# Optimization experiments

Measured on AMD Instinct MI355X. Metric: run time of the kernel, lower is better.

## Reference

```python
import jax, jax.numpy as jnp
import numpy as np

B, T, C = 4, 1024, 1024
H, G = 16, 1            # n_head, n_query_groups
D = C // H              # head_dim = 64
E, K = 4, 1             # moe_num_experts, moe_k
FF = 4 * C              # ffn/expert hidden = 4096
EPS = 1e-5


def setup_inputs() -> dict:
    key = jax.random.key(0)
    ks = jax.random.split(key, 24)
    w = lambda k, shape: (jax.random.normal(k, shape, jnp.float32) * 0.02)
    return {
        "x": jax.random.normal(ks[0], (B, T, C), jnp.float32),
        # attention (torch Linear weights stored as [in, out])
        "wq": w(ks[1], (C, C)), "wk": w(ks[2], (C, C)), "wv": w(ks[3], (C, C)),
        "wo": w(ks[4], (C, C)), "bo": jnp.zeros((C,), jnp.float32),
        # feedforward
        "ff_w1": w(ks[5], (C, FF)), "ff_b1": jnp.zeros((FF,), jnp.float32),
        "ff_w2": w(ks[6], (FF, C)), "ff_b2": jnp.zeros((C,), jnp.float32),
        # MoE experts (stacked) + gate
        "exp_w1": w(ks[7], (E, C, FF)), "exp_b1": jnp.zeros((E, FF), jnp.float32),
        "exp_w2": w(ks[8], (E, FF, C)), "exp_b2": jnp.zeros((E, C), jnp.float32),
        "gate_w": w(ks[9], (C, E)), "gate_b": jnp.zeros((E,), jnp.float32),
        # layernorms
        "ln1_g": jnp.ones((C,), jnp.float32), "ln1_b": jnp.zeros((C,), jnp.float32),
        "ln2_g": jnp.ones((C,), jnp.float32), "ln2_b": jnp.zeros((C,), jnp.float32),
        "ln3_g": jnp.ones((C,), jnp.float32), "ln3_b": jnp.zeros((C,), jnp.float32),
    }


def _ln(x, g, b):
    m = x.mean(-1, keepdims=True)
    v = x.var(-1, keepdims=True)
    return (x - m) / jnp.sqrt(v + EPS) * g + b


def reference(x, wq, wk, wv, wo, bo, ff_w1, ff_b1, ff_w2, ff_b2,
              exp_w1, exp_b1, exp_w2, exp_b2, gate_w, gate_b,
              ln1_g, ln1_b, ln2_g, ln2_b, ln3_g, ln3_b):
    Hg = H // G
    # ---- grouped-query causal self-attention ----
    h = _ln(x, ln1_g, ln1_b)
    # [B,T,C] -> [B,G,Hg,T,D]
    q = (h @ wq).reshape(B, T, G, Hg, D).transpose(0, 2, 3, 1, 4)
    k = (h @ wk).reshape(B, T, G, Hg, D).transpose(0, 2, 3, 1, 4)
    v = (h @ wv).reshape(B, T, G, Hg, D).transpose(0, 2, 3, 1, 4)
    scores = jnp.einsum('bghtd,bghsd->bghts', q, k) / np.float32(np.sqrt(D))
    causal = jnp.tril(jnp.ones((T, T), bool))
    scores = jnp.where(causal, scores, -jnp.inf)
    probs = jax.nn.softmax(scores, axis=-1)
    o = jnp.einsum('bghts,bghsd->bghtd', probs, v)          # [B,G,Hg,T,D]
    o = o.reshape(B, H, T, D).transpose(0, 2, 1, 3).reshape(B, T, C)
    x = x + o @ wo + bo
    # ---- dense feedforward ----
    h = _ln(x, ln2_g, ln2_b)
    x = x + jax.nn.relu(h @ ff_w1 + ff_b1) @ ff_w2 + ff_b2
    # ---- MoE: compute ALL experts densely, gather top-k (faithful to source) ----
    h = _ln(x, ln3_g, ln3_b)
    gate = h @ gate_w + gate_b                               # [B,T,E]
    topk_s, topk_i = jax.lax.top_k(gate, K)                  # [B,T,K]
    topk_w = jax.nn.softmax(topk_s, axis=-1)
    hidden = jax.nn.relu(jnp.einsum('btc,ech->bteh', h, exp_w1) + exp_b1)
    expert_out = jnp.einsum('bteh,ehc->btec', hidden, exp_w2) + exp_b2  # [B,T,E,C]
    sel = jnp.take_along_axis(expert_out, topk_i[..., None], axis=2)    # [B,T,K,C]
    moe = (sel * topk_w[..., None]).sum(axis=2)
    return x + moe
```

## Files before the change

### kernel.cpp

```cpp
#include <hip/hip_runtime.h>


using f16   = _Float16;
using f16x4 = __attribute__((ext_vector_type(4))) _Float16;
using f16x8 = __attribute__((ext_vector_type(8))) _Float16;
using f32x4 = __attribute__((ext_vector_type(4))) float;

__device__ __forceinline__ void async16(void* l, const void* g) {
  __builtin_amdgcn_global_load_lds(
      (const __attribute__((address_space(1))) unsigned*)g,
      (__attribute__((address_space(3))) unsigned*)l, 16, 0, 0);
}

template <bool SPLITW>
__global__ __launch_bounds__(256) void transpose_k(
    const float* __restrict__ in, f16* __restrict__ oh, f16* __restrict__ ol,
    int R, int Cc) {
  const size_t bofs = (size_t)blockIdx.y * R * Cc;
  in += bofs; oh += bofs;
  if constexpr (SPLITW) ol += bofs;
  __shared__ float tile[32][33];
  const int nbx = Cc >> 5;
  const int bx = blockIdx.x % nbx, by = blockIdx.x / nbx;
  const int tx = threadIdx.x & 31, ty = threadIdx.x >> 5;
#pragma unroll
  for (int i = 0; i < 4; ++i) {
    int r = ty + i * 8;
    tile[r][tx] = in[(size_t)(by * 32 + r) * Cc + bx * 32 + tx];
  }
  __syncthreads();
#pragma unroll
  for (int i = 0; i < 4; ++i) {
    int oc = ty + i * 8;
    float v = tile[tx][oc];
    size_t o = (size_t)(bx * 32 + oc) * R + by * 32 + tx;
    f16 hi = (f16)v;
    oh[o] = hi;
    if constexpr (SPLITW) ol[o] = (f16)(v - (float)hi);
  }
}

__global__ __launch_bounds__(256) void ln_k(
    const float* __restrict__ x, const float* __restrict__ g,
    const float* __restrict__ b, f16* __restrict__ outh, f16* __restrict__ outl) {
  const int row = blockIdx.x;
  const float4 vv = ((const float4*)(x + (size_t)row * 1024))[threadIdx.x];
  float s = vv.x + vv.y + vv.z + vv.w;
  float sq = vv.x * vv.x + vv.y * vv.y + vv.z * vv.z + vv.w * vv.w;
#pragma unroll
  for (int mm = 32; mm; mm >>= 1) { s += __shfl_xor(s, mm); sq += __shfl_xor(sq, mm); }
  __shared__ float red[8];
  const int wv = threadIdx.x >> 6;
  if ((threadIdx.x & 63) == 0) { red[wv] = s; red[4 + wv] = sq; }
  __syncthreads();
  s = red[0] + red[1] + red[2] + red[3];
  sq = red[4] + red[5] + red[6] + red[7];
  const float mean = s * 0.0009765625f;
  const float rstd = rsqrtf(sq * 0.0009765625f - mean * mean + 1e-5f);
  const int c = threadIdx.x * 4;
  const float xs[4] = {vv.x, vv.y, vv.z, vv.w};
  f16x4 ovh, ovl;
#pragma unroll
  for (int i = 0; i < 4; ++i) {
    float val = (xs[i] - mean) * rstd * g[c + i] + b[c + i];
    f16 hi = (f16)val;
    ovh[i] = hi;
    ovl[i] = (f16)(val - (float)hi);
  }
  *(f16x4*)(outh + (size_t)row * 1024 + c) = ovh;
  *(f16x4*)(outl + (size_t)row * 1024 + c) = ovl;
}

__global__ __launch_bounds__(256) void gate_k(
    const float* __restrict__ x, const float* __restrict__ g, const float* __restrict__ b,
    const float* __restrict__ gw, const float* __restrict__ gb,
    int* __restrict__ cnt, int* __restrict__ idxAll, int* __restrict__ eid) {
  const int t = blockIdx.x;
  const float4 vv = ((const float4*)(x + (size_t)t * 1024))[threadIdx.x];
  float s = vv.x + vv.y + vv.z + vv.w;
  float sq = vv.x * vv.x + vv.y * vv.y + vv.z * vv.z + vv.w * vv.w;
#pragma unroll
  for (int mm = 32; mm; mm >>= 1) { s += __shfl_xor(s, mm); sq += __shfl_xor(sq, mm); }
  __shared__ float red[8];
  __shared__ float redv[4][4];
  const int wv = threadIdx.x >> 6;
  if ((threadIdx.x & 63) == 0) { red[wv] = s; red[4 + wv] = sq; }
  __syncthreads();
  s = red[0] + red[1] + red[2] + red[3];
  sq = red[4] + red[5] + red[6] + red[7];
  const float mean = s * 0.0009765625f;
  const float rstd = rsqrtf(sq * 0.0009765625f - mean * mean + 1e-5f);
  const int c = threadIdx.x * 4;
  const float xs[4] = {vv.x, vv.y, vv.z, vv.w};
  float a0 = 0.f, a1 = 0.f, a2 = 0.f, a3 = 0.f;
#pragma unroll
  for (int i = 0; i < 4; ++i) {
    float ln = (xs[i] - mean) * rstd * g[c + i] + b[c + i];
    const float4 w4 = ((const float4*)gw)[c + i];
    a0 += ln * w4.x; a1 += ln * w4.y; a2 += ln * w4.z; a3 += ln * w4.w;
  }
#pragma unroll
  for (int mm = 32; mm; mm >>= 1) {
    a0 += __shfl_xor(a0, mm); a1 += __shfl_xor(a1, mm);
    a2 += __shfl_xor(a2, mm); a3 += __shfl_xor(a3, mm);
  }
  if ((threadIdx.x & 63) == 0) {
    redv[wv][0] = a0; redv[wv][1] = a1; redv[wv][2] = a2; redv[wv][3] = a3;
  }
  __syncthreads();
  if (threadIdx.x == 0) {
    float ge[4];
#pragma unroll
    for (int e = 0; e < 4; ++e)
      ge[e] = redv[0][e] + redv[1][e] + redv[2][e] + redv[3][e] + gb[e];
    int be = 0; float bvv = ge[0];
#pragma unroll
    for (int e = 1; e < 4; ++e) if (ge[e] > bvv) { bvv = ge[e]; be = e; }
    int pos = atomicAdd(&cnt[be], 1);
    idxAll[(be << 12) + pos] = t;
    eid[t] = be;
  }
}

__global__ void init_moe(int* cnt) { if (threadIdx.x < 4) cnt[threadIdx.x] = 0; }

#define MAXMT 36
__global__ void plan_k(const int* __restrict__ cnt, int* __restrict__ desc) {
  if (threadIdx.x == 0) {
    int t = 0;
    for (int e = 0; e < 4; ++e) {
      const int c = cnt[e];
      for (int m = 0; m < c; m += 128) desc[t++] = (e << 16) | (m >> 7);
    }
    for (; t < MAXMT; ++t) desc[t] = -1;
  }
}

template <bool MOE>
__global__ __launch_bounds__(256) void reduce_k(
    const float* __restrict__ p0, const float* __restrict__ p1,
    const float* __restrict__ res, const float* __restrict__ bias,
    const int* __restrict__ eid, float* __restrict__ o) {
  const int row = blockIdx.x, t = threadIdx.x;
  const float* bp = MOE ? bias + (size_t)eid[row] * 1024 : bias;
  const float4 a = ((const float4*)(p0 + (size_t)row * 1024))[t];
  const float4 b = ((const float4*)(p1 + (size_t)row * 1024))[t];
  const float4 r = ((const float4*)(res + (size_t)row * 1024))[t];
  const float4 bb = ((const float4*)bp)[t];
  float4 o4;
  o4.x = r.x + a.x + b.x + bb.x;
  o4.y = r.y + a.y + b.y + bb.y;
  o4.z = r.z + a.z + b.z + bb.z;
  o4.w = r.w + a.w + b.w + bb.w;
  ((float4*)(o + (size_t)row * 1024))[t] = o4;
}

template <bool SPLIT, bool RELU, bool BIAS, bool RES, bool GATHER, int OUT,
          bool QKV3, bool KSPLIT>
__global__ __launch_bounds__(256, 2) void gemm_k(
    const f16* __restrict__ Ah, const f16* __restrict__ Al,
    const f16* __restrict__ Bh, const f16* __restrict__ Bl,
    float* __restrict__ outf, float* __restrict__ outf2,
    f16* __restrict__ outh, f16* __restrict__ outl,
    const float* __restrict__ bias, const float* __restrict__ res,
    const int* __restrict__ idxAll, const int* __restrict__ cntAll,
    const int* __restrict__ desc,
    int M, int N, int K) {
  const int NB = N >> 7;
  int m0, n0, ks = 0;
  int cnt = M;
  const int* idx = nullptr;
  if constexpr (GATHER) {
    int rem = blockIdx.x;
    if constexpr (KSPLIT) {
      const int half = (int)gridDim.x >> 1;
      ks = rem >= half; rem -= ks * half;
    }
    const int mt = rem / NB, nt = rem - mt * NB;
    const int d = desc[mt];
    if (d < 0) return;
    const int e = d >> 16;
    m0 = (d & 0xffff) << 7;
    n0 = nt << 7;
    cnt = cntAll[e];
    idx = idxAll + (e << 12);
    Bh += (size_t)e * N * K;
    if (BIAS) bias += (size_t)e * N;
  } else {
    int rem = blockIdx.x;
    const int ntile = (int)gridDim.x >> (KSPLIT ? 1 : 0);
    if constexpr (KSPLIT) { ks = rem >= ntile; rem -= ks * ntile; }
    const int q2 = ntile >> 3;
    const int bid = (rem & 7) * q2 + (rem >> 3);
    m0 = (bid / NB) << 7; n0 = (bid % NB) << 7;
  }

  __shared__ __align__(16) char lds[65536];

  const int tid = threadIdx.x;
  const int wave = tid >> 6, lane = tid & 63;
  const int wr = (wave >> 1) << 6, wc = (wave & 1) << 6;
  const int srow = lane >> 3;
  const int lc = (lane & 7) ^ srow;
  const int kofs = (SPLIT ? (lc >> 1) : lc) << 4;

  const int kshift = (KSPLIT && ks) ? (K >> 1) : 0;

  const char* srcA[4];
  const char* srcB[4];
#pragma unroll
  for (int s = 0; s < 4; ++s) {
    const int tr = (wave * 4 + s) * 8 + srow;
    int gm = m0 + tr;
    if constexpr (GATHER) gm = idx[gm < cnt ? gm : cnt - 1];
    const f16* baseA = (SPLIT && (lc & 1)) ? Al : Ah;
    srcA[s] = (const char*)baseA + ((size_t)gm * K + kshift) * 2 + kofs;
    const f16* baseB = (SPLIT && (lc & 1)) ? Bl : Bh;
    srcB[s] = (const char*)baseB + ((size_t)(n0 + tr) * K + kshift) * 2 + kofs;
  }
  char* const ldsw = lds + wave * 4096;

  const int s4 = lane >> 4, l7 = lane & 7, fr = lane & 15;
  int offAh[4], offAl[4], offBh[4], offBl[4];
#pragma unroll
  for (int i = 0; i < 4; ++i) {
    const int row = wr + i * 16 + fr;
    const int col = wc + i * 16 + fr;
    if constexpr (SPLIT) {
      offAh[i] = row * 128 + (((2 * s4) ^ l7) << 4);
      offAl[i] = row * 128 + (((2 * s4 + 1) ^ l7) << 4);
      offBh[i] = 16384 + col * 128 + (((2 * s4) ^ l7) << 4);
      offBl[i] = 16384 + col * 128 + (((2 * s4 + 1) ^ l7) << 4);
    } else {
      offAh[i] = row * 128 + ((s4 ^ l7) << 4);
      offAl[i] = row * 128 + (((4 + s4) ^ l7) << 4);
      offBh[i] = 16384 + col * 128 + ((s4 ^ l7) << 4);
      offBl[i] = 16384 + col * 128 + (((4 + s4) ^ l7) << 4);
    }
  }

  f32x4 acc[4][4] = {};

  constexpr int KSTEP = SPLIT ? 32 : 64;
  const int nt_ = (KSPLIT ? (K >> 1) : K) / KSTEP;

#pragma unroll
  for (int s = 0; s < 4; ++s) {
    async16(ldsw + s * 1024, srcA[s]);
    async16(ldsw + 16384 + s * 1024, srcB[s]);
  }

  for (int t = 0; t < nt_; ++t) {
    const int cur = t & 1;
    if (t + 1 < nt_) {
      const size_t kb = (size_t)(t + 1) * (KSTEP * 2);
      char* dst = ldsw + (cur ^ 1) * 32768;
#pragma unroll
      for (int s = 0; s < 4; ++s) {
        async16(dst + s * 1024, srcA[s] + kb);
        async16(dst + 16384 + s * 1024, srcB[s] + kb);
      }
      asm volatile("s_waitcnt vmcnt(8)" ::: "memory");
    } else {
      asm volatile("s_waitcnt vmcnt(0)" ::: "memory");
    }
    __builtin_amdgcn_s_barrier();
    __builtin_amdgcn_sched_barrier(0);

    const char* cab = lds + cur * 32768;
    f16x8 va[4], vb[4], va2[4], vb2[4];
#pragma unroll
    for (int i = 0; i < 4; ++i) {
      va[i]  = *(const f16x8*)(cab + offAh[i]);
      va2[i] = *(const f16x8*)(cab + offAl[i]);
      vb[i]  = *(const f16x8*)(cab + offBh[i]);
      vb2[i] = *(const f16x8*)(cab + offBl[i]);
    }
    __builtin_amdgcn_s_setprio(1);
#pragma unroll
    for (int i = 0; i < 4; ++i)
#pragma unroll
      for (int j = 0; j < 4; ++j) {
        if constexpr (SPLIT) {
          acc[i][j] = __builtin_amdgcn_mfma_f32_16x16x32_f16(va[i],  vb[j],  acc[i][j], 0, 0, 0);
          acc[i][j] = __builtin_amdgcn_mfma_f32_16x16x32_f16(va2[i], vb[j],  acc[i][j], 0, 0, 0);
          acc[i][j] = __builtin_amdgcn_mfma_f32_16x16x32_f16(va[i],  vb2[j], acc[i][j], 0, 0, 0);
        } else {
          acc[i][j] = __builtin_amdgcn_mfma_f32_16x16x32_f16(va[i],  vb[j],  acc[i][j], 0, 0, 0);
          acc[i][j] = __builtin_amdgcn_mfma_f32_16x16x32_f16(va2[i], vb2[j], acc[i][j], 0, 0, 0);
        }
      }
    __builtin_amdgcn_s_setprio(0);
    __builtin_amdgcn_sched_barrier(0);
    __builtin_amdgcn_s_barrier();
  }

  const int cl = lane & 15, rg = lane >> 4;
  float* const po = (OUT == 3) ? (ks ? outf2 : outf) : outf;
#pragma unroll
  for (int i = 0; i < 4; ++i) {
#pragma unroll
    for (int r = 0; r < 4; ++r) {
      const int mloc = m0 + wr + i * 16 + rg * 4 + r;
      if (GATHER && mloc >= cnt) continue;
      const int orow = GATHER ? idx[mloc] : mloc;
#pragma unroll
      for (int j = 0; j < 4; ++j) {
        const int col = n0 + wc + j * 16 + cl;
        float v2 = acc[i][j][r];
        if (BIAS) v2 += bias[col];
        if (RELU) v2 = v2 > 0.f ? v2 : 0.f;
        if (RES) v2 += res[(size_t)orow * N + col];
        size_t oidx;
        if constexpr (QKV3) oidx = ((size_t)(col >> 10) * M + orow) * 1024 + (col & 1023);
        else oidx = (size_t)orow * N + col;
        if constexpr (OUT == 0 || OUT == 3) {
          po[oidx] = v2;
        } else if constexpr (OUT == 1) {
          f16 hi = (f16)v2;
          outh[oidx] = hi;
          outl[oidx] = (f16)(v2 - (float)hi);
        } else {
          outh[oidx] = (f16)v2;
        }
      }
    }
  }
}

__global__ __launch_bounds__(256, 2) void attn_k(
    const f16* __restrict__ qh, const f16* __restrict__ ql,
    const f16* __restrict__ kh, const f16* __restrict__ kl,
    const f16* __restrict__ vh, const f16* __restrict__ vl,
    f16* __restrict__ oh, f16* __restrict__ ol) {
  const int qt = blockIdx.x & 15, hd = (blockIdx.x >> 4) & 15, bb = blockIdx.x >> 8;
  const int tid = threadIdx.x, wave = tid >> 6, lane = tid & 63;
  __shared__ __align__(16) char Qs[16384], Ks[16384], Vs[16384], Ps[16384];
  const int swz = (((lane & 7) ^ ((lane >> 3) & 7)) << 4);
  const size_t tok0 = (size_t)bb * 1024;
  const int hoff = hd * 64;
  const float L2E = 1.44269504089f;

#pragma unroll
  for (int r = 0; r < 2; ++r) {
    const int chunk = wave * 2 + r;
    const int row = chunk * 8 + (lane >> 3);
    const size_t byte = (((tok0 + qt * 64 + row) * 1024 + hoff) << 1) + swz;
    async16(Qs + chunk * 1024, (const char*)qh + byte);
    async16(Qs + 8192 + chunk * 1024, (const char*)ql + byte);
  }

  f32x4 oacc[4] = {};
  float mrun[4] = {-1e30f, -1e30f, -1e30f, -1e30f};
  float lrun[4] = {};

  for (int kt = 0; kt <= qt; ++kt) {
    __syncthreads();
#pragma unroll
    for (int r = 0; r < 2; ++r) {
      const int chunk = wave * 2 + r;
      const int row = chunk * 8 + (lane >> 3);
      const size_t byte = (((tok0 + kt * 64 + row) * 1024 + hoff) << 1) + swz;
      async16(Ks + chunk * 1024, (const char*)kh + byte);
      async16(Ks + 8192 + chunk * 1024, (const char*)kl + byte);
    }
    {
      const int kv = tid >> 2, d0 = (tid & 3) << 4;
      const size_t vbase = (tok0 + kt * 64 + kv) * 1024 + hoff + d0;
      f16x8 a0 = *(const f16x8*)(vh + vbase);
      f16x8 a1 = *(const f16x8*)(vh + vbase + 8);
      f16x8 c0 = *(const f16x8*)(vl + vbase);
      f16x8 c1 = *(const f16x8*)(vl + vbase + 8);
#pragma unroll
      for (int jj = 0; jj < 8; ++jj) {
        const int d = d0 + jj, d2 = d0 + 8 + jj;
        const int o1 = d * 128 + ((kv * 2) ^ ((d & 7) << 4));
        const int o2 = d2 * 128 + ((kv * 2) ^ ((d2 & 7) << 4));
        *(f16*)(Vs + o1) = a0[jj]; *(f16*)(Vs + 8192 + o1) = c0[jj];
        *(f16*)(Vs + o2) = a1[jj]; *(f16*)(Vs + 8192 + o2) = c1[jj];
      }
    }
    __syncthreads();

    f32x4 s[4] = {};
#pragma unroll
    for (int ks = 0; ks < 2; ++ks) {
      const int qrow = wave * 16 + (lane & 15);
      const int qoff = qrow * 128 + ((((ks << 2) + (lane >> 4)) ^ (qrow & 7)) << 4);
      f16x8 a_h = *(const f16x8*)(Qs + qoff);
      f16x8 a_l = *(const f16x8*)(Qs + 8192 + qoff);
#pragma unroll
      for (int j = 0; j < 4; ++j) {
        const int col = j * 16 + (lane & 15);
        const int koff = col * 128 + ((((ks << 2) + (lane >> 4)) ^ (col & 7)) << 4);
        f16x8 b_h = *(const f16x8*)(Ks + koff);
        f16x8 b_l = *(const f16x8*)(Ks + 8192 + koff);
        s[j] = __builtin_amdgcn_mfma_f32_16x16x32_f16(a_h, b_h, s[j], 0, 0, 0);
        s[j] = __builtin_amdgcn_mfma_f32_16x16x32_f16(a_l, b_h, s[j], 0, 0, 0);
        s[j] = __builtin_amdgcn_mfma_f32_16x16x32_f16(a_h, b_l, s[j], 0, 0, 0);
      }
    }

    const bool diag = (kt == qt);
    float pmax[4] = {-1e30f, -1e30f, -1e30f, -1e30f};
#pragma unroll
    for (int j = 0; j < 4; ++j)
#pragma unroll
      for (int r = 0; r < 4; ++r) {
        float sv = s[j][r] * 0.125f;
        if (diag) {
          const int qloc = wave * 16 + (lane >> 4) * 4 + r;
          const int kvl = j * 16 + (lane & 15);
          if (kvl > qloc) sv = -1e30f;
        }
        s[j][r] = sv;
        pmax[r] = fmaxf(pmax[r], sv);
      }
    char* pbh = Ps + wave * 2048;
    char* pbl = Ps + 8192 + wave * 2048;
#pragma unroll
    for (int r = 0; r < 4; ++r) {
#pragma unroll
      for (int mm = 1; mm < 16; mm <<= 1)
        pmax[r] = fmaxf(pmax[r], __shfl_xor(pmax[r], mm, 16));
      const float mnew = fmaxf(mrun[r], pmax[r]);
      const float al = exp2f((mrun[r] - mnew) * L2E);
      mrun[r] = mnew;
      lrun[r] *= al;
      oacc[0][r] *= al; oacc[1][r] *= al; oacc[2][r] *= al; oacc[3][r] *= al;
    }

    float psum[4] = {};
#pragma unroll
    for (int j = 0; j < 4; ++j)
#pragma unroll
      for (int r = 0; r < 4; ++r) {
        const float p = exp2f((s[j][r] - mrun[r]) * L2E);
        psum[r] += p;
        const int lr = (lane >> 4) * 4 + r;
        const int kvl = j * 16 + (lane & 15);
        const int poff = lr * 128 + ((kvl * 2) ^ ((lr & 7) << 4));
        f16 ph = (f16)p;
        *(f16*)(pbh + poff) = ph;
        *(f16*)(pbl + poff) = (f16)(p - (float)ph);
      }
#pragma unroll
    for (int r = 0; r < 4; ++r) {
#pragma unroll
      for (int mm = 1; mm < 16; mm <<= 1)
        psum[r] += __shfl_xor(psum[r], mm, 16);
      lrun[r] += psum[r];
    }

#pragma unroll
    for (int ks = 0; ks < 2; ++ks) {
      const int prow = lane & 15;
      const int poff = prow * 128 + ((((ks << 2) + (lane >> 4)) ^ (prow & 7)) << 4);
      f16x8 a_h = *(const f16x8*)(pbh + poff);
      f16x8 a_l = *(const f16x8*)(pbl + poff);
#pragma unroll
      for (int jd = 0; jd < 4; ++jd) {
        const int col = jd * 16 + (lane & 15);
        const int voff = col * 128 + ((((ks << 2) + (lane >> 4)) ^ (col & 7)) << 4);
        f16x8 b_h = *(const f16x8*)(Vs + voff);
        f16x8 b_l = *(const f16x8*)(Vs + 8192 + voff);
        oacc[jd] = __builtin_amdgcn_mfma_f32_16x16x32_f16(a_h, b_h, oacc[jd], 0, 0, 0);
        oacc[jd] = __builtin_amdgcn_mfma_f32_16x16x32_f16(a_l, b_h, oacc[jd], 0, 0, 0);
        oacc[jd] = __builtin_amdgcn_mfma_f32_16x16x32_f16(a_h, b_l, oacc[jd], 0, 0, 0);
      }
    }
  }

#pragma unroll
  for (int r = 0; r < 4; ++r) {
    const float inv = 1.0f / lrun[r];
    const size_t trow = tok0 + qt * 64 + wave * 16 + (lane >> 4) * 4 + r;
#pragma unroll
    for (int jd = 0; jd < 4; ++jd) {
      const int col = hoff + jd * 16 + (lane & 15);
      const float val = oacc[jd][r] * inv;
      const f16 hi = (f16)val;
      oh[trow * 1024 + col] = hi;
      ol[trow * 1024 + col] = (f16)(val - (float)hi);
    }
  }
}

extern "C" void kernel_launch(void* const* d_in, const int* in_sizes, int n_in,
                              void* d_out, int out_size, void* d_ws, size_t ws_size,
                              hipStream_t stream) {
  const float* x0   = (const float*)d_in[0];
  const float* wq   = (const float*)d_in[1];
  const float* wk   = (const float*)d_in[2];
  const float* wv   = (const float*)d_in[3];
  const float* wo   = (const float*)d_in[4];
  const float* bo   = (const float*)d_in[5];
  const float* ffw1 = (const float*)d_in[6];
  const float* ffb1 = (const float*)d_in[7];
  const float* ffw2 = (const float*)d_in[8];
  const float* ffb2 = (const float*)d_in[9];
  const float* ew1  = (const float*)d_in[10];
  const float* eb1  = (const float*)d_in[11];
  const float* ew2  = (const float*)d_in[12];
  const float* eb2  = (const float*)d_in[13];
  const float* gw   = (const float*)d_in[14];
  const float* gb   = (const float*)d_in[15];
  const float* l1g  = (const float*)d_in[16];
  const float* l1b  = (const float*)d_in[17];
  const float* l2g  = (const float*)d_in[18];
  const float* l2b  = (const float*)d_in[19];
  const float* l3g  = (const float*)d_in[20];
  const float* l3b  = (const float*)d_in[21];
  float* out = (float*)d_out;

  char* w = (char*)d_ws;
  const size_t M1 = (size_t)1024 * 1024;
  const size_t A1 = (size_t)4096 * 1024 * 2;
  const size_t W4 = (size_t)1024 * 4096 * 2;
  f16* wqkvh = (f16*)w; w += 3 * M1 * 2;
  f16* wqkvl = (f16*)w; w += 3 * M1 * 2;
  f16* woh = (f16*)w; w += M1 * 2;
  f16* wol = (f16*)w; w += M1 * 2;
  f16* f1h = (f16*)w; w += W4;  f16* f1l = (f16*)w; w += W4;
  f16* f2h = (f16*)w; w += W4;  f16* f2l = (f16*)w; w += W4;
  f16* e1t = (f16*)w; w += 4 * W4;
  f16* e2t = (f16*)w; w += 4 * W4;
  f16* hh  = (f16*)w; w += A1;  f16* hl  = (f16*)w; w += A1;
  f16* qkv_h = (f16*)w; w += 3 * A1;
  f16* qkv_l = (f16*)w; w += 3 * A1;
  f16* o_h = (f16*)w; w += A1;  f16* o_l = (f16*)w; w += A1;
  float* x1 = (float*)w; w += (size_t)4096 * 1024 * 4;
  int* cnt = (int*)w; w += 256;
  int* idx = (int*)w; w += (size_t)4 * 4096 * 4;
  int* eid = (int*)w; w += (size_t)4096 * 4;
  int* desc = (int*)w; w += 256;
  f16* hid_h = qkv_h;
  f16* hid_l = (f16*)((char*)qkv_h + (((size_t)32) << 20));
  f16* ffh   = qkv_h;
  float* pW0 = (float*)hh;
  float* pW1 = (float*)qkv_h;
  float* pF0 = (float*)wqkvh;
  float* pF1 = (float*)hh;
  float* pM0 = (float*)((char*)qkv_l + (((size_t)8) << 20));
  float* pM1 = (float*)o_h;

  transpose_k<true><<<1024, 256, 0, stream>>>(wq, wqkvh, wqkvl, 1024, 1024);
  transpose_k<true><<<1024, 256, 0, stream>>>(wk, wqkvh + M1, wqkvl + M1, 1024, 1024);
  transpose_k<true><<<1024, 256, 0, stream>>>(wv, wqkvh + 2 * M1, wqkvl + 2 * M1, 1024, 1024);
  transpose_k<true><<<1024, 256, 0, stream>>>(wo, woh, wol, 1024, 1024);
  transpose_k<true><<<4096, 256, 0, stream>>>(ffw1, f1h, f1l, 1024, 4096);
  transpose_k<true><<<4096, 256, 0, stream>>>(ffw2, f2h, f2l, 4096, 1024);
  transpose_k<false><<<dim3(4096, 4), 256, 0, stream>>>(ew1, e1t, nullptr, 1024, 4096);
  transpose_k<false><<<dim3(4096, 4), 256, 0, stream>>>(ew2, e2t, nullptr, 4096, 1024);

  const size_t TOK = (size_t)4096 * 1024;
  ln_k<<<4096, 256, 0, stream>>>(x0, l1g, l1b, hh, hl);
  gemm_k<true, false, false, false, false, 1, true, false><<<768, 256, 0, stream>>>(
      hh, hl, wqkvh, wqkvl, nullptr, nullptr, qkv_h, qkv_l,
      nullptr, nullptr, nullptr, nullptr, nullptr, 4096, 3072, 1024);
  attn_k<<<1024, 256, 0, stream>>>(qkv_h, qkv_l, qkv_h + TOK, qkv_l + TOK,
                                   qkv_h + 2 * TOK, qkv_l + 2 * TOK, o_h, o_l);
  gemm_k<true, false, false, false, false, 3, false, true><<<512, 256, 0, stream>>>(
      o_h, o_l, woh, wol, pW0, pW1, nullptr, nullptr,
      nullptr, nullptr, nullptr, nullptr, nullptr, 4096, 1024, 1024);
  reduce_k<false><<<4096, 256, 0, stream>>>(pW0, pW1, x0, bo, nullptr, x1);

  ln_k<<<4096, 256, 0, stream>>>(x1, l2g, l2b, hh, hl);
  gemm_k<true, true, true, false, false, 1, false, false><<<1024, 256, 0, stream>>>(
      hh, hl, f1h, f1l, nullptr, nullptr, hid_h, hid_l,
      ffb1, nullptr, nullptr, nullptr, nullptr, 4096, 4096, 1024);
  gemm_k<true, false, false, false, false, 3, false, true><<<512, 256, 0, stream>>>(
      hid_h, hid_l, f2h, f2l, pF0, pF1, nullptr, nullptr,
      nullptr, nullptr, nullptr, nullptr, nullptr, 4096, 1024, 4096);
  reduce_k<false><<<4096, 256, 0, stream>>>(pF0, pF1, x1, ffb2, nullptr, out);

  ln_k<<<4096, 256, 0, stream>>>(out, l3g, l3b, hh, hl);
  init_moe<<<1, 64, 0, stream>>>(cnt);
  gate_k<<<4096, 256, 0, stream>>>(out, l3g, l3b, gw, gb, cnt, idx, eid);
  plan_k<<<1, 64, 0, stream>>>(cnt, desc);
  gemm_k<false, true, true, false, true, 2, false, false><<<MAXMT * 32, 256, 0, stream>>>(
      hh, nullptr, e1t, nullptr, nullptr, nullptr, ffh, nullptr,
      eb1, nullptr, idx, cnt, desc, 4096, 4096, 1024);
  gemm_k<false, false, false, false, true, 3, false, true><<<2 * MAXMT * 8, 256, 0, stream>>>(
      ffh, nullptr, e2t, nullptr, pM0, pM1, nullptr, nullptr,
      nullptr, nullptr, idx, cnt, desc, 4096, 1024, 4096);
  reduce_k<true><<<4096, 256, 0, stream>>>(pM0, pM1, out, eb2, eid, out);
}
```

Measured before the change: 789.0 us.

## Pre-transpose V in QKV epilogue, hoist Q to registers, reuse LDS for P

The QKV GEMM epilogue now writes V in a per-head transposed layout ([b,h,d,t]). Attention can then load V tiles with async global-to-LDS copies instead of scalar transposing stores. Q fragments are loaded into registers once, which frees the Q LDS buffer to be reused for P. That cuts LDS from 64KB to 48KB, enabling 3 blocks per CU, and the q-tile order is reversed so the longest causal tiles are scheduled first. Risks include strided scattered writes in the GEMM epilogue for V and higher register pressure under the tighter launch bound.

```diff
diff --git a/kernel.cpp b/kernel.cpp
--- a/kernel.cpp
+++ b/kernel.cpp
@@ -312,8 +312,18 @@
         if (RELU) v2 = v2 > 0.f ? v2 : 0.f;
         if (RES) v2 += res[(size_t)orow * N + col];
         size_t oidx;
-        if constexpr (QKV3) oidx = ((size_t)(col >> 10) * M + orow) * 1024 + (col & 1023);
-        else oidx = (size_t)orow * N + col;
+        if constexpr (QKV3) {
+          if (col < 2048) {
+            oidx = ((size_t)(col >> 10) * M + orow) * 1024 + (col & 1023);
+          } else {
+            const int c = col - 2048;
+            oidx = (size_t)2 * M * 1024 +
+                   (((size_t)(orow >> 10) * 16 + (c >> 6)) * 64 + (c & 63)) * 1024 +
+                   (orow & 1023);
+          }
+        } else {
+          oidx = (size_t)orow * N + col;
+        }
         if constexpr (OUT == 0 || OUT == 3) {
           po[oidx] = v2;
         } else if constexpr (OUT == 1) {
@@ -328,17 +338,18 @@
   }
 }
 
-__global__ __launch_bounds__(256, 2) void attn_k(
+__global__ __launch_bounds__(256, 3) void attn_k(
     const f16* __restrict__ qh, const f16* __restrict__ ql,
     const f16* __restrict__ kh, const f16* __restrict__ kl,
-    const f16* __restrict__ vh, const f16* __restrict__ vl,
+    const f16* __restrict__ vth, const f16* __restrict__ vtl,
     f16* __restrict__ oh, f16* __restrict__ ol) {
-  const int qt = blockIdx.x & 15, hd = (blockIdx.x >> 4) & 15, bb = blockIdx.x >> 8;
+  const int qt = 15 - (blockIdx.x & 15), hd = (blockIdx.x >> 4) & 15, bb = blockIdx.x >> 8;
   const int tid = threadIdx.x, wave = tid >> 6, lane = tid & 63;
-  __shared__ __align__(16) char Qs[16384], Ks[16384], Vs[16384], Ps[16384];
+  __shared__ __align__(16) char QPs[16384], Ks[16384], Vs[16384];
   const int swz = (((lane & 7) ^ ((lane >> 3) & 7)) << 4);
   const size_t tok0 = (size_t)bb * 1024;
   const int hoff = hd * 64;
+  const size_t vbase = ((size_t)(bb * 16 + hd) * 64) * 1024;
   const float L2E = 1.44269504089f;
 
 #pragma unroll
@@ -346,8 +357,17 @@
     const int chunk = wave * 2 + r;
     const int row = chunk * 8 + (lane >> 3);
     const size_t byte = (((tok0 + qt * 64 + row) * 1024 + hoff) << 1) + swz;
-    async16(Qs + chunk * 1024, (const char*)qh + byte);
-    async16(Qs + 8192 + chunk * 1024, (const char*)ql + byte);
+    async16(QPs + chunk * 1024, (const char*)qh + byte);
+    async16(QPs + 8192 + chunk * 1024, (const char*)ql + byte);
+  }
+  __syncthreads();
+  f16x8 qr_h[2], qr_l[2];
+#pragma unroll
+  for (int ks = 0; ks < 2; ++ks) {
+    const int qrow = wave * 16 + (lane & 15);
+    const int qoff = qrow * 128 + ((((ks << 2) + (lane >> 4)) ^ (qrow & 7)) << 4);
+    qr_h[ks] = *(const f16x8*)(QPs + qoff);
+    qr_l[ks] = *(const f16x8*)(QPs + 8192 + qoff);
   }
 
   f32x4 oacc[4] = {};
@@ -360,44 +380,27 @@
     for (int r = 0; r < 2; ++r) {
       const int chunk = wave * 2 + r;
       const int row = chunk * 8 + (lane >> 3);
-      const size_t byte = (((tok0 + kt * 64 + row) * 1024 + hoff) << 1) + swz;
-      async16(Ks + chunk * 1024, (const char*)kh + byte);
-      async16(Ks + 8192 + chunk * 1024, (const char*)kl + byte);
-    }
-    {
-      const int kv = tid >> 2, d0 = (tid & 3) << 4;
-      const size_t vbase = (tok0 + kt * 64 + kv) * 1024 + hoff + d0;
-      f16x8 a0 = *(const f16x8*)(vh + vbase);
-      f16x8 a1 = *(const f16x8*)(vh + vbase + 8);
-      f16x8 c0 = *(const f16x8*)(vl + vbase);
-      f16x8 c1 = *(const f16x8*)(vl + vbase + 8);
-#pragma unroll
-      for (int jj = 0; jj < 8; ++jj) {
-        const int d = d0 + jj, d2 = d0 + 8 + jj;
-        const int o1 = d * 128 + ((kv * 2) ^ ((d & 7) << 4));
-        const int o2 = d2 * 128 + ((kv * 2) ^ ((d2 & 7) << 4));
-        *(f16*)(Vs + o1) = a0[jj]; *(f16*)(Vs + 8192 + o1) = c0[jj];
-        *(f16*)(Vs + o2) = a1[jj]; *(f16*)(Vs + 8192 + o2) = c1[jj];
-      }
+      const size_t kbyte = (((tok0 + kt * 64 + row) * 1024 + hoff) << 1) + swz;
+      async16(Ks + chunk * 1024, (const char*)kh + kbyte);
+      async16(Ks + 8192 + chunk * 1024, (const char*)kl + kbyte);
+      const size_t vbyte = (((vbase + (size_t)row * 1024) + kt * 64) << 1) + swz;
+      async16(Vs + chunk * 1024, (const char*)vth + vbyte);
+      async16(Vs + 8192 + chunk * 1024, (const char*)vtl + vbyte);
     }
     __syncthreads();
 
     f32x4 s[4] = {};
 #pragma unroll
     for (int ks = 0; ks < 2; ++ks) {
-      const int qrow = wave * 16 + (lane & 15);
-      const int qoff = qrow * 128 + ((((ks << 2) + (lane >> 4)) ^ (qrow & 7)) << 4);
-      f16x8 a_h = *(const f16x8*)(Qs + qoff);
-      f16x8 a_l = *(const f16x8*)(Qs + 8192 + qoff);
 #pragma unroll
       for (int j = 0; j < 4; ++j) {
         const int col = j * 16 + (lane & 15);
         const int koff = col * 128 + ((((ks << 2) + (lane >> 4)) ^ (col & 7)) << 4);
         f16x8 b_h = *(const f16x8*)(Ks + koff);
         f16x8 b_l = *(const f16x8*)(Ks + 8192 + koff);
-        s[j] = __builtin_amdgcn_mfma_f32_16x16x32_f16(a_h, b_h, s[j], 0, 0, 0);
-        s[j] = __builtin_amdgcn_mfma_f32_16x16x32_f16(a_l, b_h, s[j], 0, 0, 0);
-        s[j] = __builtin_amdgcn_mfma_f32_16x16x32_f16(a_h, b_l, s[j], 0, 0, 0);
+        s[j] = __builtin_amdgcn_mfma_f32_16x16x32_f16(qr_h[ks], b_h, s[j], 0, 0, 0);
+        s[j] = __builtin_amdgcn_mfma_f32_16x16x32_f16(qr_l[ks], b_h, s[j], 0, 0, 0);
+        s[j] = __builtin_amdgcn_mfma_f32_16x16x32_f16(qr_h[ks], b_l, s[j], 0, 0, 0);
       }
     }
 
@@ -416,8 +419,8 @@
         s[j][r] = sv;
         pmax[r] = fmaxf(pmax[r], sv);
       }
-    char* pbh = Ps + wave * 2048;
-    char* pbl = Ps + 8192 + wave * 2048;
+    char* pbh = QPs + wave * 2048;
+    char* pbl = QPs + 8192 + wave * 2048;
 #pragma unroll
     for (int r = 0; r < 4; ++r) {
 #pragma unroll
```

Result: no change. 793.1 us (+0.5%).
